# Kernel tuning notes

Hardware: AMD Instinct MI355X
Metric: run time of the kernel (lower is better)

## Reference

```python
import jax, jax.numpy as jnp
import numpy as np
from jax import lax

SRS = (250, 500, 1000)
LCM = 1000
INSERTION_STEPS = tuple(LCM // sr for sr in SRS)  # (4, 2, 1)
KERNEL = LCM // 200  # lcm / f_min = 5
D_MODEL = 256


def setup_inputs() -> dict:
    key = jax.random.key(0)
    k1, k2, k3, k4, k5 = jax.random.split(key, 5)
    T = 60  # seconds
    return {
        "x_250": jax.random.normal(k1, (T * 250,), jnp.float32),
        "x_500": jax.random.normal(k2, (T * 500,), jnp.float32),
        "x_1000": jax.random.normal(k3, (T * 1000,), jnp.float32),
        "W": jax.random.normal(k4, (D_MODEL, 1, KERNEL), jnp.float32) * 0.1,
        "b": jax.random.normal(k5, (D_MODEL,), jnp.float32) * 0.1,
    }


def reference(x_250, x_500, x_1000, W, b):
    xs = [x_250, x_500, x_1000]
    steps = list(INSERTION_STEPS)
    lens = [int(x.shape[0]) for x in xs]
    L = lens[0] * steps[0]            # common upsampled length (= T * lcm)
    max_len = max(lens)

    # strided zero-fill upsample -> [n_streams, 1, L]
    X_up = jnp.zeros((len(xs), 1, L), dtype=xs[0].dtype)
    for i, (x, s) in enumerate(zip(xs, steps)):
        X_up = X_up.at[i, 0, ::s].set(x)

    # Conv1d(in=1, out=d_model, 'same' padding, odd kernel)
    pad = (KERNEL - 1) // 2
    Y = lax.conv_general_dilated(
        X_up, W, window_strides=(1,), padding=[(pad, pad)],
        dimension_numbers=("NCH", "OIH", "NCH"),
    ) + b[None, :, None]              # [n_streams, d_model, L]

    # gather back original sample positions (mask==1 cols), zero-pad to max_len
    pos = jnp.arange(max_len)
    outs = []
    for i, (s, l) in enumerate(zip(steps, lens)):
        idx = jnp.clip(pos * s, 0, L - 1)          # [max_len]
        g = Y[i][:, idx]                            # [d_model, max_len]
        outs.append(jnp.where((pos < l)[None, :], g, jnp.zeros((), Y.dtype)))
    X = jnp.stack(outs)                             # [n_streams, d_model, max_len]

    # S: nonzero (row, col) indices of mask M, each padded/truncated to max_len
    rows = jnp.concatenate([jnp.full((l,), i, jnp.int32) for i, l in enumerate(lens)])
    cols = jnp.concatenate([jnp.arange(l, dtype=jnp.int32) * s for s, l in zip(steps, lens)])
    total = sum(lens)
    if total < max_len:
        rows = jnp.pad(rows, (0, max_len - total))
        cols = jnp.pad(cols, (0, max_len - total))
    S = jnp.stack([rows[:max_len], cols[:max_len]])  # [2, max_len]
    return X, S
```

## Files before the change

kernel.cpp:

```cpp
#include <hip/hip_runtime.h>
#include <hip/hip_bf16.h>


#define L_OUT   60000
#define LEN0    15000
#define LEN1    30000
#define LEN2    60000
#define DMODEL  256
#define X_ELEMS (3 * DMODEL * L_OUT)

typedef float float4v __attribute__((ext_vector_type(4)));

__device__ __forceinline__ void st4(float* p, float a, float b, float c, float d) {
    float4v v; v.x = a; v.y = b; v.z = c; v.w = d;
    *(float4v*)p = v;
}

__device__ __forceinline__ float ld_or_zero(const float* __restrict__ x,
                                            int idx, int len) {
    return (idx >= 0 && idx < len) ? x[idx] : 0.0f;
}

__global__ __launch_bounds__(256) void embed_kernel(
    const float* __restrict__ x250,
    const float* __restrict__ x500,
    const float* __restrict__ x1000,
    const float* __restrict__ W,
    const float* __restrict__ b,
    float* __restrict__ out)
{
    const int chunk = blockIdx.x;
    const int cg    = blockIdx.y;
    const int i     = blockIdx.z;
    const int tid   = threadIdx.x;

    if (cg == 8) {
        const int sid = i * 59 + chunk;
        const int t0  = sid * 1024 + tid * 4;
        if (t0 >= 2 * L_OUT) return;
        float ov[4];
#pragma unroll
        for (int j = 0; j < 4; ++j) {
            const int t = t0 + j;
            float val;
            if (t < L_OUT) {
                val = (t < 15000) ? 0.0f : ((t < 45000) ? 1.0f : 2.0f);
            } else {
                const int u = t - L_OUT;
                int iv;
                if (u < 15000)      iv = 4 * u;
                else if (u < 45000) iv = 2 * (u - 15000);
                else                iv = u - 45000;
                val = (float)iv;
            }
            ov[j] = val;
        }
        st4(out + X_ELEMS + t0, ov[0], ov[1], ov[2], ov[3]);
        return;
    }

    const int p0 = chunk * 1024 + tid * 4;
    if (p0 >= L_OUT) return;

    const int cbase = cg * 32;
    float* dst = out + (size_t)(i * DMODEL + cbase) * L_OUT + p0;
    const int len = (i == 0) ? LEN0 : (i == 1) ? LEN1 : LEN2;

    if (p0 >= len) {
#pragma unroll 4
        for (int ci = 0; ci < 32; ++ci) { st4(dst, 0.f, 0.f, 0.f, 0.f); dst += L_OUT; }
        return;
    }

    if (i == 0) {
        float xv[4];
#pragma unroll
        for (int j = 0; j < 4; ++j) xv[j] = x250[p0 + j];
#pragma unroll 4
        for (int ci = 0; ci < 32; ++ci) {
            const int c = cbase + ci;
            const float w2 = W[c * 5 + 2], bias = b[c];
            float y[4];
#pragma unroll
            for (int j = 0; j < 4; ++j) y[j] = fmaf(w2, xv[j], bias);
            st4(dst, y[0], y[1], y[2], y[3]);
            dst += L_OUT;
        }
    } else if (i == 1) {
        float a[6];
#pragma unroll
        for (int j = 0; j < 6; ++j) a[j] = ld_or_zero(x500, p0 - 1 + j, LEN1);
#pragma unroll 4
        for (int ci = 0; ci < 32; ++ci) {
            const int c = cbase + ci;
            const float w0 = W[c * 5 + 0], w2 = W[c * 5 + 2],
                        w4 = W[c * 5 + 4], bias = b[c];
            float y[4];
#pragma unroll
            for (int j = 0; j < 4; ++j) {
                float acc = fmaf(w0, a[j], bias);
                acc = fmaf(w2, a[j + 1], acc);
                acc = fmaf(w4, a[j + 2], acc);
                y[j] = acc;
            }
            st4(dst, y[0], y[1], y[2], y[3]);
            dst += L_OUT;
        }
    } else {
        float a[8];
#pragma unroll
        for (int j = 0; j < 8; ++j) a[j] = ld_or_zero(x1000, p0 - 2 + j, LEN2);
#pragma unroll 4
        for (int ci = 0; ci < 32; ++ci) {
            const int c = cbase + ci;
            const float w0 = W[c * 5 + 0], w1 = W[c * 5 + 1], w2 = W[c * 5 + 2],
                        w3 = W[c * 5 + 3], w4 = W[c * 5 + 4], bias = b[c];
            float y[4];
#pragma unroll
            for (int j = 0; j < 4; ++j) {
                float acc = fmaf(w0, a[j], bias);
                acc = fmaf(w1, a[j + 1], acc);
                acc = fmaf(w2, a[j + 2], acc);
                acc = fmaf(w3, a[j + 3], acc);
                acc = fmaf(w4, a[j + 4], acc);
                y[j] = acc;
            }
            st4(dst, y[0], y[1], y[2], y[3]);
            dst += L_OUT;
        }
    }
}

extern "C" void kernel_launch(void* const* d_in, const int* in_sizes, int n_in,
                              void* d_out, int out_size, void* d_ws, size_t ws_size,
                              hipStream_t stream) {
    const float* x250  = (const float*)d_in[0];
    const float* x500  = (const float*)d_in[1];
    const float* x1000 = (const float*)d_in[2];
    const float* W     = (const float*)d_in[3];
    const float* b     = (const float*)d_in[4];
    float* out = (float*)d_out;

    dim3 grid(59, 9, 3);
    embed_kernel<<<grid, 256, 0, stream>>>(x250, x500, x1000, W, b, out);
}
```

Baseline: 186.9 us.

## Remap work so each block writes half an output row contiguously

Replaces the 3D grid (position chunk × 32-channel group × stream) with a 1D grid where each block handles half of one channel row and loops over positions with float4 vector loads of the input. Weights are loaded once per block, and each block's stores form one long contiguous streaming run instead of a strided walk across 32 rows. The index tail is written by 30 blocks that each cover four 256-float4 chunks. The cost is more redundant input loads per output (neighbouring float4s) and fewer, longer blocks, which may change load balance.

```diff
diff --git a/kernel.cpp b/kernel.cpp
--- a/kernel.cpp
+++ b/kernel.cpp
@@ -8,17 +8,13 @@
 #define LEN2    60000
 #define DMODEL  256
 #define X_ELEMS (3 * DMODEL * L_OUT)
+#define HALF4   7500
 
 typedef float float4v __attribute__((ext_vector_type(4)));
 
 __device__ __forceinline__ void st4(float* p, float a, float b, float c, float d) {
     float4v v; v.x = a; v.y = b; v.z = c; v.w = d;
     *(float4v*)p = v;
-}
-
-__device__ __forceinline__ float ld_or_zero(const float* __restrict__ x,
-                                            int idx, int len) {
-    return (idx >= 0 && idx < len) ? x[idx] : 0.0f;
 }
 
 __global__ __launch_bounds__(256) void embed_kernel(
@@ -29,104 +25,99 @@
     const float* __restrict__ b,
     float* __restrict__ out)
 {
-    const int chunk = blockIdx.x;
-    const int cg    = blockIdx.y;
-    const int i     = blockIdx.z;
-    const int tid   = threadIdx.x;
+    const int bid = blockIdx.x;
+    const int tid = threadIdx.x;
 
-    if (cg == 8) {
-        const int sid = i * 59 + chunk;
-        const int t0  = sid * 1024 + tid * 4;
-        if (t0 >= 2 * L_OUT) return;
-        float ov[4];
+    if (bid >= 1536) {
+        const int s = bid - 1536;
+        const int base = s * 1024;
 #pragma unroll
         for (int j = 0; j < 4; ++j) {
-            const int t = t0 + j;
-            float val;
-            if (t < L_OUT) {
-                val = (t < 15000) ? 0.0f : ((t < 45000) ? 1.0f : 2.0f);
-            } else {
-                const int u = t - L_OUT;
-                int iv;
-                if (u < 15000)      iv = 4 * u;
-                else if (u < 45000) iv = 2 * (u - 15000);
-                else                iv = u - 45000;
-                val = (float)iv;
+            const int q4 = base + j * 256 + tid;
+            if (q4 < 30000) {
+                float ov[4];
+#pragma unroll
+                for (int k = 0; k < 4; ++k) {
+                    const int e = q4 * 4 + k;
+                    float val;
+                    if (e < L_OUT) {
+                        val = (e < 15000) ? 0.0f : ((e < 45000) ? 1.0f : 2.0f);
+                    } else {
+                        const int u = e - L_OUT;
+                        int iv;
+                        if (u < 15000)      iv = 4 * u;
+                        else if (u < 45000) iv = 2 * (u - 15000);
+                        else                iv = u - 45000;
+                        val = (float)iv;
+                    }
+                    ov[k] = val;
+                }
+                st4(out + X_ELEMS + q4 * 4, ov[0], ov[1], ov[2], ov[3]);
             }
-            ov[j] = val;
         }
-        st4(out + X_ELEMS + t0, ov[0], ov[1], ov[2], ov[3]);
         return;
     }
 
-    const int p0 = chunk * 1024 + tid * 4;
-    if (p0 >= L_OUT) return;
+    const int row  = bid >> 1;
+    const int half = bid & 1;
+    const int i    = row >> 8;
+    const int c    = row & 255;
 
-    const int cbase = cg * 32;
-    float* dst = out + (size_t)(i * DMODEL + cbase) * L_OUT + p0;
-    const int len = (i == 0) ? LEN0 : (i == 1) ? LEN1 : LEN2;
+    float* __restrict__ dstrow = out + (size_t)row * L_OUT;
 
-    if (p0 >= len) {
-#pragma unroll 4
-        for (int ci = 0; ci < 32; ++ci) { st4(dst, 0.f, 0.f, 0.f, 0.f); dst += L_OUT; }
+    if (half == 1 && i != 2) {
+        float* d = dstrow + 30000;
+        for (int p4l = tid; p4l < HALF4; p4l += 256)
+            st4(d + p4l * 4, 0.f, 0.f, 0.f, 0.f);
         return;
     }
 
+    const float w0 = W[c * 5 + 0], w1 = W[c * 5 + 1], w2 = W[c * 5 + 2],
+                w3 = W[c * 5 + 3], w4 = W[c * 5 + 4], bias = b[c];
+
     if (i == 0) {
-        float xv[4];
-#pragma unroll
-        for (int j = 0; j < 4; ++j) xv[j] = x250[p0 + j];
-#pragma unroll 4
-        for (int ci = 0; ci < 32; ++ci) {
-            const int c = cbase + ci;
-            const float w2 = W[c * 5 + 2], bias = b[c];
-            float y[4];
-#pragma unroll
-            for (int j = 0; j < 4; ++j) y[j] = fmaf(w2, xv[j], bias);
-            st4(dst, y[0], y[1], y[2], y[3]);
-            dst += L_OUT;
+        const float4v* __restrict__ x4 = (const float4v*)x250;
+        for (int p4 = tid; p4 < HALF4; p4 += 256) {
+            if (p4 < 3750) {
+                const float4v xv = x4[p4];
+                st4(dstrow + p4 * 4,
+                    fmaf(w2, xv.x, bias), fmaf(w2, xv.y, bias),
+                    fmaf(w2, xv.z, bias), fmaf(w2, xv.w, bias));
+            } else {
+                st4(dstrow + p4 * 4, 0.f, 0.f, 0.f, 0.f);
+            }
         }
     } else if (i == 1) {
-        float a[6];
-#pragma unroll
-        for (int j = 0; j < 6; ++j) a[j] = ld_or_zero(x500, p0 - 1 + j, LEN1);
-#pragma unroll 4
-        for (int ci = 0; ci < 32; ++ci) {
-            const int c = cbase + ci;
-            const float w0 = W[c * 5 + 0], w2 = W[c * 5 + 2],
-                        w4 = W[c * 5 + 4], bias = b[c];
-            float y[4];
-#pragma unroll
-            for (int j = 0; j < 4; ++j) {
-                float acc = fmaf(w0, a[j], bias);
-                acc = fmaf(w2, a[j + 1], acc);
-                acc = fmaf(w4, a[j + 2], acc);
-                y[j] = acc;
-            }
-            st4(dst, y[0], y[1], y[2], y[3]);
-            dst += L_OUT;
+        const float4v* __restrict__ x4 = (const float4v*)x500;
+        const float4v z4 = {0.f, 0.f, 0.f, 0.f};
+        for (int p4 = tid; p4 < HALF4; p4 += 256) {
+            const float4v lo  = (p4 > 0)    ? x4[p4 - 1] : z4;
+            const float4v mid = x4[p4];
+            const float4v hi  = (p4 < 7499) ? x4[p4 + 1] : z4;
+            float y0 = fmaf(w0, lo.w,  bias); y0 = fmaf(w2, mid.x, y0); y0 = fmaf(w4, mid.y, y0);
+            float y1 = fmaf(w0, mid.x, bias); y1 = fmaf(w2, mid.y, y1); y1 = fmaf(w4, mid.z, y1);
+            float y2 = fmaf(w0, mid.y, bias); y2 = fmaf(w2, mid.z, y2); y2 = fmaf(w4, mid.w, y2);
+            float y3 = fmaf(w0, mid.z, bias); y3 = fmaf(w2, mid.w, y3); y3 = fmaf(w4, hi.x,  y3);
+            st4(dstrow + p4 * 4, y0, y1, y2, y3);
         }
     } else {
-        float a[8];
-#pragma unroll
-        for (int j = 0; j < 8; ++j) a[j] = ld_or_zero(x1000, p0 - 2 + j, LEN2);
-#pragma unroll 4
-        for (int ci = 0; ci < 32; ++ci) {
-            const int c = cbase + ci;
-            const float w0 = W[c * 5 + 0], w1 = W[c * 5 + 1], w2 = W[c * 5 + 2],
-                        w3 = W[c * 5 + 3], w4 = W[c * 5 + 4], bias = b[c];
-            float y[4];
-#pragma unroll
-            for (int j = 0; j < 4; ++j) {
-                float acc = fmaf(w0, a[j], bias);
-                acc = fmaf(w1, a[j + 1], acc);
-                acc = fmaf(w2, a[j + 2], acc);
-                acc = fmaf(w3, a[j + 3], acc);
-                acc = fmaf(w4, a[j + 4], acc);
-                y[j] = acc;
-            }
-            st4(dst, y[0], y[1], y[2], y[3]);
-            dst += L_OUT;
+        const float4v* __restrict__ x4 = (const float4v*)x1000;
+        const float4v z4 = {0.f, 0.f, 0.f, 0.f};
+        const int p4base = half * HALF4;
+        for (int p4l = tid; p4l < HALF4; p4l += 256) {
+            const int p4 = p4base + p4l;
+            const float4v lo  = (p4 > 0)     ? x4[p4 - 1] : z4;
+            const float4v mid = x4[p4];
+            const float4v hi  = (p4 < 14999) ? x4[p4 + 1] : z4;
+            float y0 = fmaf(w0, lo.z,  bias); y0 = fmaf(w1, lo.w,  y0);
+            y0 = fmaf(w2, mid.x, y0);  y0 = fmaf(w3, mid.y, y0);  y0 = fmaf(w4, mid.z, y0);
+            float y1 = fmaf(w0, lo.w,  bias); y1 = fmaf(w1, mid.x, y1);
+            y1 = fmaf(w2, mid.y, y1);  y1 = fmaf(w3, mid.z, y1);  y1 = fmaf(w4, mid.w, y1);
+            float y2 = fmaf(w0, mid.x, bias); y2 = fmaf(w1, mid.y, y2);
+            y2 = fmaf(w2, mid.z, y2);  y2 = fmaf(w3, mid.w, y2);  y2 = fmaf(w4, hi.x,  y2);
+            float y3 = fmaf(w0, mid.y, bias); y3 = fmaf(w1, mid.z, y3);
+            y3 = fmaf(w2, mid.w, y3);  y3 = fmaf(w3, hi.x,  y3);  y3 = fmaf(w4, hi.y,  y3);
+            st4(dstrow + p4 * 4, y0, y1, y2, y3);
         }
     }
 }
@@ -141,6 +132,6 @@
     const float* b     = (const float*)d_in[4];
     float* out = (float*)d_out;
 
-    dim3 grid(59, 9, 3);
+    dim3 grid(1566, 1, 1);
     embed_kernel<<<grid, 256, 0, stream>>>(x250, x500, x1000, W, b, out);
 }
```

Measured after the change: 204.3 us. +9.3%, slower.
